# Kernel tuning notes

Hardware: AMD Instinct MI355X
Metric: run time of the kernel (lower is better)

Reference implementation:

```python
import jax, jax.numpy as jnp
import numpy as np

N_NODES = 50000
N_EDGES = 800000
IN_DIM = 256
HID = 64
HEADS = [4, 4, 1]
N_CLASSES = 16
SLOPE = 0.2


def mish(x):
    return x * jnp.tanh(jax.nn.softplus(x))


def gat_conv(x, src, dst, W, attn_l, attn_r, bias, res_W, n_heads, d_out, act):
    """DGL GATConv (feat_drop=attn_drop=0, residual=True, bias=True).
    x: (N, F_in); src/dst: (E,) edge endpoints; message flows src -> dst.
    """
    N = x.shape[0]
    feat = (x @ W).reshape(N, n_heads, d_out)            # (N, H, D)
    el = jnp.sum(feat * attn_l, axis=-1)                 # (N, H)
    er = jnp.sum(feat * attn_r, axis=-1)                 # (N, H)
    e = jax.nn.leaky_relu(el[src] + er[dst], SLOPE)      # (E, H)
    # segment softmax over incoming edges of each dst node
    emax = jax.ops.segment_max(e, dst, num_segments=N)   # (N, H)
    ee = jnp.exp(e - emax[dst])                          # (E, H)
    denom = jax.ops.segment_sum(ee, dst, num_segments=N) # (N, H)
    a = ee / denom[dst]                                  # (E, H)
    # weighted scatter-aggregate of source features
    rst = jax.ops.segment_sum(feat[src] * a[:, :, None], dst, num_segments=N)  # (N, H, D)
    # residual: identity if F_in == H*D else linear projection (DGL semantics)
    if res_W is None:
        res = x.reshape(N, n_heads, d_out)
    else:
        res = (x @ res_W).reshape(N, n_heads, d_out)
    rst = rst + res + bias.reshape(1, n_heads, d_out)
    if act:
        rst = mish(rst)
    return rst


def setup_inputs() -> dict:
    key = jax.random.key(0)
    ks = jax.random.split(key, 16)
    x = jax.random.normal(ks[0], (N_NODES, IN_DIM), dtype=jnp.float32)
    src = jax.random.randint(ks[1], (N_EDGES,), 0, N_NODES, dtype=jnp.int32)
    dst = jax.random.randint(ks[2], (N_EDGES,), 0, N_NODES, dtype=jnp.int32)
    s = 0.1
    # layer 0: 256 -> 4 heads x 64
    W0 = jax.random.normal(ks[3], (IN_DIM, HEADS[0] * HID), jnp.float32) * s
    al0 = jax.random.normal(ks[4], (HEADS[0], HID), jnp.float32) * s
    ar0 = jax.random.normal(ks[5], (HEADS[0], HID), jnp.float32) * s
    b0 = jnp.zeros((HEADS[0] * HID,), jnp.float32)
    # layer 1: 256 -> 4 heads x 64
    W1 = jax.random.normal(ks[6], (HEADS[0] * HID, HEADS[1] * HID), jnp.float32) * s
    al1 = jax.random.normal(ks[7], (HEADS[1], HID), jnp.float32) * s
    ar1 = jax.random.normal(ks[8], (HEADS[1], HID), jnp.float32) * s
    b1 = jnp.zeros((HEADS[1] * HID,), jnp.float32)
    # output layer: 256 -> 1 head x 16 (residual needs a linear projection)
    W2 = jax.random.normal(ks[9], (HEADS[1] * HID, HEADS[2] * N_CLASSES), jnp.float32) * s
    al2 = jax.random.normal(ks[10], (HEADS[2], N_CLASSES), jnp.float32) * s
    ar2 = jax.random.normal(ks[11], (HEADS[2], N_CLASSES), jnp.float32) * s
    b2 = jnp.zeros((HEADS[2] * N_CLASSES,), jnp.float32)
    resW2 = jax.random.normal(ks[12], (HEADS[1] * HID, HEADS[2] * N_CLASSES), jnp.float32) * s
    return {"x": x, "src": src, "dst": dst,
            "W0": W0, "al0": al0, "ar0": ar0, "b0": b0,
            "W1": W1, "al1": al1, "ar1": ar1, "b1": b1,
            "W2": W2, "al2": al2, "ar2": ar2, "b2": b2, "resW2": resW2}


def reference(x, src, dst, W0, al0, ar0, b0, W1, al1, ar1, b1, W2, al2, ar2, b2, resW2):
    N = x.shape[0]
    h = gat_conv(x, src, dst, W0, al0, ar0, b0, None, HEADS[0], HID, True).reshape(N, -1)
    h = gat_conv(h, src, dst, W1, al1, ar1, b1, None, HEADS[1], HID, True).reshape(N, -1)
    logits = gat_conv(h, src, dst, W2, al2, ar2, b2, resW2, HEADS[2], N_CLASSES, False).mean(axis=1)
    return logits
```

## Files before the change

### kernel.cpp

```cpp
#include <hip/hip_runtime.h>
#include <cmath>
#include <type_traits>

typedef __bf16 bf16;
typedef __attribute__((ext_vector_type(8))) __bf16 bf16x8;
typedef __attribute__((ext_vector_type(4))) __bf16 bf16x4;
typedef __attribute__((ext_vector_type(4))) float f32x4;

__device__ __forceinline__ unsigned f2s(float x) {
    unsigned u = __float_as_uint(x);
    return (u & 0x80000000u) ? ~u : (u | 0x80000000u);
}
__device__ __forceinline__ float s2f(unsigned s) {
    return (s & 0x80000000u) ? __uint_as_float(s & 0x7FFFFFFFu)
                             : __uint_as_float(~s);
}

__global__ void prep_weights_kernel(const float* __restrict__ W0, const float* __restrict__ W1,
                                    const float* __restrict__ W2, const float* __restrict__ rW2,
                                    bf16* __restrict__ Wt0, bf16* __restrict__ Wt1,
                                    bf16* __restrict__ Bct) {
    const int idx = blockIdx.x * blockDim.x + threadIdx.x;
    if (idx < 65536) {
        const int k = idx >> 8, m = idx & 255;
        Wt0[m * 256 + k] = (bf16)W0[idx];
        Wt1[m * 256 + k] = (bf16)W1[idx];
    }
    if (idx < 8192) {
        const int m = idx >> 8, k = idx & 255;
        const float v = (m < 16) ? W2[k * 16 + m] : rW2[k * 16 + (m - 16)];
        Bct[idx] = (bf16)v;
    }
}

template <typename AT>
__global__ __launch_bounds__(256) void gemm_mfma_bf16(const AT* __restrict__ A,
                                                      const bf16* __restrict__ Bt,
                                                      bf16* __restrict__ Fb, int N) {
    constexpr int K = 256, BM = 128, BK = 32;
    constexpr int LDA = BK + 8;
    __shared__ bf16 As[BM * LDA];
    __shared__ bf16 Bs[BM * LDA];

    const int tid = threadIdx.x;
    const int wave = tid >> 6, lane = tid & 63;
    const int quad = lane >> 4, l16 = lane & 15;
    const int rowBase = blockIdx.y * BM;
    const int colBase = blockIdx.x * BM;
    const int m_base = (wave >> 1) * 64, n_base = (wave & 1) * 64;

    f32x4 acc[4][4] = {};

    const int sr = tid >> 1;
    const int seg = (tid & 1) << 4;

    for (int k0 = 0; k0 < K; k0 += BK) {
        {
            const int gr = rowBase + sr;
            if constexpr (std::is_same<AT, float>::value) {
                float4 f0 = {0,0,0,0}, f1 = {0,0,0,0}, f2 = {0,0,0,0}, f3 = {0,0,0,0};
                if (gr < N) {
                    const float4* Ag = (const float4*)(A + (long)gr * K + k0 + seg);
                    f0 = Ag[0]; f1 = Ag[1]; f2 = Ag[2]; f3 = Ag[3];
                }
                bf16x8 p0, p1;
                p0[0] = (bf16)f0.x; p0[1] = (bf16)f0.y; p0[2] = (bf16)f0.z; p0[3] = (bf16)f0.w;
                p0[4] = (bf16)f1.x; p0[5] = (bf16)f1.y; p0[6] = (bf16)f1.z; p0[7] = (bf16)f1.w;
                p1[0] = (bf16)f2.x; p1[1] = (bf16)f2.y; p1[2] = (bf16)f2.z; p1[3] = (bf16)f2.w;
                p1[4] = (bf16)f3.x; p1[5] = (bf16)f3.y; p1[6] = (bf16)f3.z; p1[7] = (bf16)f3.w;
                *(bf16x8*)&As[sr * LDA + seg] = p0;
                *(bf16x8*)&As[sr * LDA + seg + 8] = p1;
            } else {
                bf16x8 p0 = {}, p1 = {};
                if (gr < N) {
                    const bf16x8* Ag = (const bf16x8*)(A + (long)gr * K + k0 + seg);
                    p0 = Ag[0]; p1 = Ag[1];
                }
                *(bf16x8*)&As[sr * LDA + seg] = p0;
                *(bf16x8*)&As[sr * LDA + seg + 8] = p1;
            }
        }
        {
            const bf16x8* Bg = (const bf16x8*)(Bt + (long)(colBase + sr) * K + k0 + seg);
            *(bf16x8*)&Bs[sr * LDA + seg] = Bg[0];
            *(bf16x8*)&Bs[sr * LDA + seg + 8] = Bg[1];
        }
        __syncthreads();

        bf16x8 af[4], bfr[4];
#pragma unroll
        for (int mi = 0; mi < 4; mi++)
            af[mi] = *(const bf16x8*)&As[(m_base + mi * 16 + l16) * LDA + quad * 8];
#pragma unroll
        for (int ni = 0; ni < 4; ni++)
            bfr[ni] = *(const bf16x8*)&Bs[(n_base + ni * 16 + l16) * LDA + quad * 8];
#pragma unroll
        for (int mi = 0; mi < 4; mi++)
#pragma unroll
            for (int ni = 0; ni < 4; ni++)
                acc[mi][ni] = __builtin_amdgcn_mfma_f32_16x16x32_bf16(af[mi], bfr[ni], acc[mi][ni], 0, 0, 0);
        __syncthreads();
    }

#pragma unroll
    for (int mi = 0; mi < 4; mi++) {
#pragma unroll
        for (int r = 0; r < 4; r++) {
            const int grow = rowBase + m_base + mi * 16 + quad * 4 + r;
            if (grow < N) {
#pragma unroll
                for (int ni = 0; ni < 4; ni++) {
                    Fb[(long)grow * 256 + colBase + n_base + ni * 16 + l16] = (bf16)acc[mi][ni][r];
                }
            }
        }
    }
}

__global__ __launch_bounds__(256) void gemm_mfma_n32(const bf16* __restrict__ A,
                                                     const bf16* __restrict__ Bt,
                                                     float* __restrict__ C, int N) {
    constexpr int K = 256, BM = 128, BK = 32;
    constexpr int LDA = BK + 8;
    __shared__ bf16 As[BM * LDA];
    __shared__ bf16 Bs[32 * LDA];

    const int tid = threadIdx.x;
    const int wave = tid >> 6, lane = tid & 63;
    const int quad = lane >> 4, l16 = lane & 15;
    const int rowBase = blockIdx.x * BM;
    const int m_base = (wave >> 1) * 64, n_base = (wave & 1) * 16;

    f32x4 acc[4] = {};

    const int sr = tid >> 1;
    const int seg = (tid & 1) << 4;

    for (int k0 = 0; k0 < K; k0 += BK) {
        {
            const int gr = rowBase + sr;
            bf16x8 p0 = {}, p1 = {};
            if (gr < N) {
                const bf16x8* Ag = (const bf16x8*)(A + (long)gr * K + k0 + seg);
                p0 = Ag[0]; p1 = Ag[1];
            }
            *(bf16x8*)&As[sr * LDA + seg] = p0;
            *(bf16x8*)&As[sr * LDA + seg + 8] = p1;
        }
        if (tid < 64) {
            const int br = tid >> 1;
            const bf16x8* Bg = (const bf16x8*)(Bt + br * K + k0 + seg);
            *(bf16x8*)&Bs[br * LDA + seg] = Bg[0];
            *(bf16x8*)&Bs[br * LDA + seg + 8] = Bg[1];
        }
        __syncthreads();

        const bf16x8 bfr = *(const bf16x8*)&Bs[(n_base + l16) * LDA + quad * 8];
#pragma unroll
        for (int mi = 0; mi < 4; mi++) {
            const bf16x8 af = *(const bf16x8*)&As[(m_base + mi * 16 + l16) * LDA + quad * 8];
            acc[mi] = __builtin_amdgcn_mfma_f32_16x16x32_bf16(af, bfr, acc[mi], 0, 0, 0);
        }
        __syncthreads();
    }

#pragma unroll
    for (int mi = 0; mi < 4; mi++) {
#pragma unroll
        for (int r = 0; r < 4; r++) {
            const int grow = rowBase + m_base + mi * 16 + quad * 4 + r;
            if (grow < N) C[(long)grow * 32 + n_base + l16] = acc[mi][r];
        }
    }
}

__global__ void el_er_node_kernel(const bf16* __restrict__ feat,
                                  const float* __restrict__ al, const float* __restrict__ ar,
                                  float* __restrict__ el, float* __restrict__ er, int N) {
    const int wid = (blockIdx.x * blockDim.x + threadIdx.x) >> 6;
    const int lane = threadIdx.x & 63;
    if (wid >= N) return;
    const bf16x4 f = ((const bf16x4*)feat)[(long)wid * 64 + lane];
    const float4 a = ((const float4*)al)[lane];
    const float4 b = ((const float4*)ar)[lane];
    const float f0 = (float)f[0], f1 = (float)f[1], f2 = (float)f[2], f3 = (float)f[3];
    float vl = f0 * a.x + f1 * a.y + f2 * a.z + f3 * a.w;
    float vr = f0 * b.x + f1 * b.y + f2 * b.z + f3 * b.w;
#pragma unroll
    for (int off = 1; off < 16; off <<= 1) {
        vl += __shfl_xor(vl, off);
        vr += __shfl_xor(vr, off);
    }
    if ((lane & 15) == 0) {
        const int h = lane >> 4;
        el[wid * 4 + h] = vl;
        er[wid * 4 + h] = vr;
    }
}

__global__ void el_er_strided16(const float* __restrict__ feat, int stride,
                                const float* __restrict__ al, const float* __restrict__ ar,
                                float* __restrict__ el, float* __restrict__ er, int N) {
    const int wid = (blockIdx.x * blockDim.x + threadIdx.x) >> 6;
    const int lane = threadIdx.x & 63;
    if (wid >= N) return;
    float vl = 0.f, vr = 0.f;
    if (lane < 16) {
        float f = feat[(long)wid * stride + lane];
        vl = f * al[lane];
        vr = f * ar[lane];
    }
#pragma unroll
    for (int off = 1; off < 16; off <<= 1) {
        vl += __shfl_xor(vl, off);
        vr += __shfl_xor(vr, off);
    }
    if (lane == 0) { el[wid] = vl; er[wid] = vr; }
}

__global__ void elmax4_kernel(const float4* __restrict__ el4, unsigned* __restrict__ elmax_u, int n4) {
    __shared__ float4 sm[256];
    float4 m = {-INFINITY, -INFINITY, -INFINITY, -INFINITY};
    for (int i = blockIdx.x * blockDim.x + threadIdx.x; i < n4; i += gridDim.x * blockDim.x) {
        const float4 v = el4[i];
        m.x = fmaxf(m.x, v.x); m.y = fmaxf(m.y, v.y);
        m.z = fmaxf(m.z, v.z); m.w = fmaxf(m.w, v.w);
    }
    sm[threadIdx.x] = m;
    __syncthreads();
    for (int off = 128; off > 0; off >>= 1) {
        if (threadIdx.x < off) {
            float4 o = sm[threadIdx.x + off];
            float4 c = sm[threadIdx.x];
            c.x = fmaxf(c.x, o.x); c.y = fmaxf(c.y, o.y);
            c.z = fmaxf(c.z, o.z); c.w = fmaxf(c.w, o.w);
            sm[threadIdx.x] = c;
        }
        __syncthreads();
    }
    if (threadIdx.x == 0) {
        const float4 r = sm[0];
        atomicMax(&elmax_u[0], f2s(r.x));
        atomicMax(&elmax_u[1], f2s(r.y));
        atomicMax(&elmax_u[2], f2s(r.z));
        atomicMax(&elmax_u[3], f2s(r.w));
    }
}


__global__ void count_deg_kernel(const int* __restrict__ dst, int* __restrict__ deg, int E) {
    const int e = blockIdx.x * blockDim.x + threadIdx.x;
    if (e >= E) return;
    atomicAdd(&deg[dst[e]], 1);
}

__global__ void scan_block_kernel(const int* __restrict__ deg, int* __restrict__ scanned,
                                  int* __restrict__ block_sums, int N) {
    __shared__ int smem[256];
    const int tid = threadIdx.x;
    const int base = blockIdx.x * 1024 + tid * 4;
    int v[4];
#pragma unroll
    for (int i = 0; i < 4; i++) v[i] = (base + i < N) ? deg[base + i] : 0;
    const int tsum = v[0] + v[1] + v[2] + v[3];
    smem[tid] = tsum;
    __syncthreads();
    int acc = tsum;
    for (int off = 1; off < 256; off <<= 1) {
        const int t = (tid >= off) ? smem[tid - off] : 0;
        __syncthreads();
        acc += t;
        smem[tid] = acc;
        __syncthreads();
    }
    if (tid == 255) block_sums[blockIdx.x] = acc;
    int run = acc - tsum;
#pragma unroll
    for (int i = 0; i < 4; i++) {
        if (base + i < N) scanned[base + i] = run;
        run += v[i];
    }
}

__global__ void scan_sums_kernel(int* __restrict__ block_sums, unsigned* __restrict__ elmax_u, int nb) {
    const int tid = threadIdx.x;
    if (tid < 12) elmax_u[tid] = f2s(-INFINITY);
    const int orig = (tid < nb) ? block_sums[tid] : 0;
    int v = orig;
#pragma unroll
    for (int off = 1; off < 64; off <<= 1) {
        const int t = __shfl_up(v, off);
        if (tid >= off) v += t;
    }
    if (tid < nb) block_sums[tid] = v - orig;
}

__global__ void apply_offsets_kernel(const int* __restrict__ scanned, const int* __restrict__ block_sums,
                                     int* __restrict__ row_ptr, int* __restrict__ cursor, int N, int E) {
    const int i = blockIdx.x * blockDim.x + threadIdx.x;
    if (i < N) {
        const int v = scanned[i] + block_sums[i >> 10];
        row_ptr[i] = v;
        cursor[i] = v;
    }
    if (i == 0) row_ptr[N] = E;
}

__global__ void scatter_kernel(const int* __restrict__ src, const int* __restrict__ dst,
                               int* __restrict__ cursor, int* __restrict__ csr_src, int E) {
    const int e = blockIdx.x * blockDim.x + threadIdx.x;
    if (e >= E) return;
    const int pos = atomicAdd(&cursor[dst[e]], 1);
    csr_src[pos] = src[e];
}

template <int H, int D, bool ACT, typename RT, typename OT>
__global__ void gat_aggregate_wave(const int* __restrict__ row_ptr, const int* __restrict__ csr_src,
                                   const float* __restrict__ el, const float* __restrict__ er,
                                   const unsigned* __restrict__ elmax_u,
                                   const bf16* __restrict__ feat,
                                   const RT* __restrict__ res, const float* __restrict__ bias,
                                   OT* __restrict__ out, int N) {
    constexpr int C = H * D;
    constexpr int V = C / 4;
    const int wave = threadIdx.x >> 6;
    const int lane = threadIdx.x & 63;
    int n = blockIdx.x * (blockDim.x >> 6) + wave;
    if (n >= N) return;
    n = __builtin_amdgcn_readfirstlane(n);
    const int h = lane >> 4;
    const bf16x4* feat4 = (const bf16x4*)feat;

    const float erd = er[n * H + h];
    float sh = s2f(elmax_u[h]) + erd;
    sh = (sh >= 0.f) ? sh : 0.2f * sh;

    float4 acc = {0.f, 0.f, 0.f, 0.f};
    float l = 0.f;
    int p = row_ptr[n];
    const int pend = row_ptr[n + 1];
    for (; p + 4 <= pend; p += 4) {
        const int s0 = csr_src[p + 0];
        const int s1 = csr_src[p + 1];
        const int s2 = csr_src[p + 2];
        const int s3 = csr_src[p + 3];
        float e0 = el[s0 * H + h] + erd;
        float e1 = el[s1 * H + h] + erd;
        float e2 = el[s2 * H + h] + erd;
        float e3 = el[s3 * H + h] + erd;
        e0 = (e0 >= 0.f) ? e0 : 0.2f * e0;
        e1 = (e1 >= 0.f) ? e1 : 0.2f * e1;
        e2 = (e2 >= 0.f) ? e2 : 0.2f * e2;
        e3 = (e3 >= 0.f) ? e3 : 0.2f * e3;
        const float w0 = __expf(e0 - sh);
        const float w1 = __expf(e1 - sh);
        const float w2 = __expf(e2 - sh);
        const float w3 = __expf(e3 - sh);
        const bf16x4 f0 = feat4[(long)s0 * V + lane];
        const bf16x4 f1 = feat4[(long)s1 * V + lane];
        const bf16x4 f2 = feat4[(long)s2 * V + lane];
        const bf16x4 f3 = feat4[(long)s3 * V + lane];
        l += w0 + w1 + w2 + w3;
        acc.x += w0 * (float)f0[0] + w1 * (float)f1[0] + w2 * (float)f2[0] + w3 * (float)f3[0];
        acc.y += w0 * (float)f0[1] + w1 * (float)f1[1] + w2 * (float)f2[1] + w3 * (float)f3[1];
        acc.z += w0 * (float)f0[2] + w1 * (float)f1[2] + w2 * (float)f2[2] + w3 * (float)f3[2];
        acc.w += w0 * (float)f0[3] + w1 * (float)f1[3] + w2 * (float)f2[3] + w3 * (float)f3[3];
    }
    for (; p < pend; ++p) {
        const int s = csr_src[p];
        float e = el[s * H + h] + erd;
        e = (e >= 0.f) ? e : 0.2f * e;
        const float w = __expf(e - sh);
        const bf16x4 f = feat4[(long)s * V + lane];
        l += w;
        acc.x += w * (float)f[0];
        acc.y += w * (float)f[1];
        acc.z += w * (float)f[2];
        acc.w += w * (float)f[3];
    }
    const float inv = (l > 0.f) ? 1.f / l : 0.f;
    acc.x *= inv; acc.y *= inv; acc.z *= inv; acc.w *= inv;

    float4 r;
    if constexpr (std::is_same<RT, float>::value) {
        r = ((const float4*)res)[(long)n * V + lane];
    } else {
        const bf16x4 rb = ((const bf16x4*)res)[(long)n * V + lane];
        r = make_float4((float)rb[0], (float)rb[1], (float)rb[2], (float)rb[3]);
    }
    const float4 bb = ((const float4*)bias)[lane];
    float v[4] = {acc.x + r.x + bb.x, acc.y + r.y + bb.y,
                  acc.z + r.z + bb.z, acc.w + r.w + bb.w};
    if (ACT) {
#pragma unroll
        for (int i = 0; i < 4; i++) {
            const float sp = (v[i] > 20.f) ? v[i] : log1pf(expf(v[i]));
            v[i] = v[i] * tanhf(sp);
        }
    }
    if constexpr (std::is_same<OT, float>::value) {
        float4 o = {v[0], v[1], v[2], v[3]};
        ((float4*)out)[(long)n * V + lane] = o;
    } else {
        bf16x4 o;
        o[0] = (bf16)v[0]; o[1] = (bf16)v[1]; o[2] = (bf16)v[2]; o[3] = (bf16)v[3];
        ((bf16x4*)out)[(long)n * V + lane] = o;
    }
}

template <bool ACT, int NPB>
__global__ void gat_aggregate_small(const int* __restrict__ row_ptr, const int* __restrict__ csr_src,
                                    const float* __restrict__ el, const float* __restrict__ er,
                                    const unsigned* __restrict__ elmax_u,
                                    const float* __restrict__ feat, int fstride,
                                    const float* __restrict__ res, int rstride,
                                    const float* __restrict__ bias, float* __restrict__ out, int N) {
    constexpr int C = 16;
    const int local = threadIdx.x % C;
    const int n = blockIdx.x * NPB + threadIdx.x / C;
    if (n >= N) return;
    const float mx = fmaxf(fmaxf(s2f(elmax_u[8]), s2f(elmax_u[9])),
                           fmaxf(s2f(elmax_u[10]), s2f(elmax_u[11])));
    const float erd = er[n];
    float sh = mx + erd;
    sh = (sh >= 0.f) ? sh : 0.2f * sh;

    float acc = 0.f, l = 0.f;
    int p = row_ptr[n];
    const int pend = row_ptr[n + 1];
    for (; p + 4 <= pend; p += 4) {
        const int s0 = csr_src[p + 0];
        const int s1 = csr_src[p + 1];
        const int s2 = csr_src[p + 2];
        const int s3 = csr_src[p + 3];
        float e0 = el[s0] + erd, e1 = el[s1] + erd, e2 = el[s2] + erd, e3 = el[s3] + erd;
        e0 = (e0 >= 0.f) ? e0 : 0.2f * e0;
        e1 = (e1 >= 0.f) ? e1 : 0.2f * e1;
        e2 = (e2 >= 0.f) ? e2 : 0.2f * e2;
        e3 = (e3 >= 0.f) ? e3 : 0.2f * e3;
        const float w0 = __expf(e0 - sh);
        const float w1 = __expf(e1 - sh);
        const float w2 = __expf(e2 - sh);
        const float w3 = __expf(e3 - sh);
        l += w0 + w1 + w2 + w3;
        acc += w0 * feat[(long)s0 * fstride + local] + w1 * feat[(long)s1 * fstride + local]
             + w2 * feat[(long)s2 * fstride + local] + w3 * feat[(long)s3 * fstride + local];
    }
    for (; p < pend; ++p) {
        const int s = csr_src[p];
        float e = el[s] + erd;
        e = (e >= 0.f) ? e : 0.2f * e;
        const float w = __expf(e - sh);
        l += w;
        acc += w * feat[(long)s * fstride + local];
    }
    const float inv = (l > 0.f) ? 1.f / l : 0.f;
    float v = acc * inv + res[(long)n * rstride + local] + bias[local];
    if (ACT) {
        const float sp = (v > 20.f) ? v : log1pf(expf(v));
        v = v * tanhf(sp);
    }
    out[(long)n * C + local] = v;
}


static inline int cdiv(long a, long b) { return (int)((a + b - 1) / b); }

extern "C" void kernel_launch(void* const* d_in, const int* in_sizes, int n_in,
                              void* d_out, int out_size, void* d_ws, size_t ws_size,
                              hipStream_t stream) {
    const float* x   = (const float*)d_in[0];
    const int*   src = (const int*)d_in[1];
    const int*   dst = (const int*)d_in[2];
    const float* W0  = (const float*)d_in[3];
    const float* al0 = (const float*)d_in[4];
    const float* ar0 = (const float*)d_in[5];
    const float* b0  = (const float*)d_in[6];
    const float* W1  = (const float*)d_in[7];
    const float* al1 = (const float*)d_in[8];
    const float* ar1 = (const float*)d_in[9];
    const float* b1  = (const float*)d_in[10];
    const float* W2  = (const float*)d_in[11];
    const float* al2 = (const float*)d_in[12];
    const float* ar2 = (const float*)d_in[13];
    const float* b2  = (const float*)d_in[14];
    const float* rW2 = (const float*)d_in[15];
    float* out = (float*)d_out;

    const int N = in_sizes[0] / 256;
    const int E = in_sizes[1];

    bf16* Wt0    = (bf16*)d_ws;
    bf16* Wt1    = Wt0 + 65536;
    bf16* Bct    = Wt1 + 65536;
    bf16* Fb     = Bct + 8192;
    bf16* Hb     = Fb + (long)N * 256;
    float* F2    = (float*)(Hb + (long)N * 256);
    float* el    = F2 + (long)N * 32;
    float* er    = el + (long)N * 4;
    unsigned* elmax_u = (unsigned*)(er + (long)N * 4);
    int* deg     = (int*)(elmax_u + 12);
    int* scanned = deg + N;
    int* bsums   = scanned + N;
    int* row_ptr = bsums + 64;
    int* cursor  = row_ptr + N + 1;
    int* csr_src = cursor + N;

    const int THREADS = 256;
    const int NB = cdiv(N, 1024);
    dim3 mfma_grid(2, cdiv(N, 128));

    prep_weights_kernel<<<cdiv(65536, THREADS), THREADS, 0, stream>>>(W0, W1, W2, rW2, Wt0, Wt1, Bct);
    hipMemsetAsync(deg, 0, (size_t)N * 4, stream);
    count_deg_kernel<<<cdiv(E, THREADS), THREADS, 0, stream>>>(dst, deg, E);
    scan_block_kernel<<<NB, 256, 0, stream>>>(deg, scanned, bsums, N);
    scan_sums_kernel<<<1, 64, 0, stream>>>(bsums, elmax_u, NB);
    apply_offsets_kernel<<<cdiv(N, THREADS), THREADS, 0, stream>>>(scanned, bsums, row_ptr, cursor, N, E);
    scatter_kernel<<<cdiv(E, THREADS), THREADS, 0, stream>>>(src, dst, cursor, csr_src, E);

    gemm_mfma_bf16<float><<<mfma_grid, 256, 0, stream>>>(x, Wt0, Fb, N);
    el_er_node_kernel<<<cdiv(N, 4), 256, 0, stream>>>(Fb, al0, ar0, el, er, N);
    elmax4_kernel<<<64, 256, 0, stream>>>((const float4*)el, elmax_u, N);
    gat_aggregate_wave<4, 64, true, float, bf16><<<cdiv(N, 4), 256, 0, stream>>>(
        row_ptr, csr_src, el, er, elmax_u, Fb, x, b0, Hb, N);

    gemm_mfma_bf16<bf16><<<mfma_grid, 256, 0, stream>>>(Hb, Wt1, Fb, N);
    el_er_node_kernel<<<cdiv(N, 4), 256, 0, stream>>>(Fb, al1, ar1, el, er, N);
    elmax4_kernel<<<64, 256, 0, stream>>>((const float4*)el, elmax_u + 4, N);
    gat_aggregate_wave<4, 64, true, bf16, bf16><<<cdiv(N, 4), 256, 0, stream>>>(
        row_ptr, csr_src, el, er, elmax_u + 4, Fb, Hb, b1, Hb, N);

    gemm_mfma_n32<<<cdiv(N, 128), 256, 0, stream>>>(Hb, Bct, F2, N);
    el_er_strided16<<<cdiv(N, 4), 256, 0, stream>>>(F2, 32, al2, ar2, el, er, N);
    elmax4_kernel<<<64, 256, 0, stream>>>((const float4*)el, elmax_u + 8, N / 4);
    gat_aggregate_small<false, 16><<<cdiv(N, 16), 256, 0, stream>>>(row_ptr, csr_src, el, er, elmax_u,
                                                                    F2, 32, F2 + 16, 32, b2, out, N);
}
```

Measured before the change: 478.4 us.

## Split edges across half-waves in GAT aggregation and use fast exp2/mish

The 256-channel aggregation now has each half-wave process alternate edges with 8-wide bf16 loads, then combines the two halves with a cross-lane shuffle. The 16-class output layer moves from 16 lanes per node to one wave per node, with four edge slots per wave reduced by shuffles. Leaky-relu plus exp is folded into a single exp2 over a max of two FMAs, and mish uses a closed-form rational expression with a hardware reciprocal. These changes target gather latency and transcendental cost. They add shuffle reductions and use 32-bit unsigned byte offsets, plus approximate math that may change rounding slightly.

```diff
diff --git a/kernel.cpp b/kernel.cpp
--- a/kernel.cpp
+++ b/kernel.cpp
@@ -14,6 +14,13 @@
 __device__ __forceinline__ float s2f(unsigned s) {
     return (s & 0x80000000u) ? __uint_as_float(s & 0x7FFFFFFFu)
                              : __uint_as_float(~s);
+}
+
+__device__ __forceinline__ float fast_mish(float x) {
+    const float t = __expf(fminf(x, 32.f));
+    const float num = fmaf(t, t, t + t);
+    const float den = num + 2.f;
+    return x * num * __builtin_amdgcn_rcpf(den);
 }
 
 __global__ void prep_weights_kernel(const float* __restrict__ W0, const float* __restrict__ W1,
@@ -321,146 +328,168 @@
                                    const bf16* __restrict__ feat,
                                    const RT* __restrict__ res, const float* __restrict__ bias,
                                    OT* __restrict__ out, int N) {
-    constexpr int C = H * D;
-    constexpr int V = C / 4;
+    static_assert(H == 4 && D == 64, "layout hardcoded for C=256");
     const int wave = threadIdx.x >> 6;
     const int lane = threadIdx.x & 63;
     int n = blockIdx.x * (blockDim.x >> 6) + wave;
     if (n >= N) return;
     n = __builtin_amdgcn_readfirstlane(n);
-    const int h = lane >> 4;
-    const bf16x4* feat4 = (const bf16x4*)feat;
+    const int sel = lane >> 5;
+    const int hl = lane & 31;
+    const int h = hl >> 3;
 
     const float erd = er[n * H + h];
     float sh = s2f(elmax_u[h]) + erd;
-    sh = (sh >= 0.f) ? sh : 0.2f * sh;
-
-    float4 acc = {0.f, 0.f, 0.f, 0.f};
+    sh = fmaxf(sh, 0.2f * sh);
+    constexpr float L2E = 1.4426950408889634f;
+    const float C1 = (erd - sh) * L2E;
+    const float C2 = fmaf(0.2f, erd, -sh) * L2E;
+
+    const char* csrB = (const char*)csr_src;
+    const char* elB = (const char*)el;
+    const char* featB = (const char*)feat;
+    const unsigned hoff = (unsigned)(h << 2);
+    const unsigned coff = (unsigned)(hl << 4);
+    const unsigned selo = (unsigned)(sel << 2);
+
+    float acc[8] = {0.f, 0.f, 0.f, 0.f, 0.f, 0.f, 0.f, 0.f};
     float l = 0.f;
     int p = row_ptr[n];
     const int pend = row_ptr[n + 1];
+
+#define EDGE2(PP)                                                                  \
+    {                                                                              \
+        const int s_ = *(const int*)(csrB + ((unsigned)((PP) << 2) + selo));       \
+        const float ev_ = *(const float*)(elB + ((unsigned)(s_ << 4) + hoff));     \
+        const float w_ = __builtin_amdgcn_exp2f(                                   \
+            fmaxf(fmaf(ev_, L2E, C1), fmaf(ev_, 0.2f * L2E, C2)));                 \
+        const bf16x8 f_ = *(const bf16x8*)(featB + ((unsigned)(s_ << 9) + coff));  \
+        l += w_;                                                                   \
+        _Pragma("unroll") for (int i_ = 0; i_ < 8; i_++)                           \
+            acc[i_] = fmaf(w_, (float)f_[i_], acc[i_]);                            \
+    }
+
     for (; p + 4 <= pend; p += 4) {
-        const int s0 = csr_src[p + 0];
-        const int s1 = csr_src[p + 1];
-        const int s2 = csr_src[p + 2];
-        const int s3 = csr_src[p + 3];
-        float e0 = el[s0 * H + h] + erd;
-        float e1 = el[s1 * H + h] + erd;
-        float e2 = el[s2 * H + h] + erd;
-        float e3 = el[s3 * H + h] + erd;
-        e0 = (e0 >= 0.f) ? e0 : 0.2f * e0;
-        e1 = (e1 >= 0.f) ? e1 : 0.2f * e1;
-        e2 = (e2 >= 0.f) ? e2 : 0.2f * e2;
-        e3 = (e3 >= 0.f) ? e3 : 0.2f * e3;
-        const float w0 = __expf(e0 - sh);
-        const float w1 = __expf(e1 - sh);
-        const float w2 = __expf(e2 - sh);
-        const float w3 = __expf(e3 - sh);
-        const bf16x4 f0 = feat4[(long)s0 * V + lane];
-        const bf16x4 f1 = feat4[(long)s1 * V + lane];
-        const bf16x4 f2 = feat4[(long)s2 * V + lane];
-        const bf16x4 f3 = feat4[(long)s3 * V + lane];
-        l += w0 + w1 + w2 + w3;
-        acc.x += w0 * (float)f0[0] + w1 * (float)f1[0] + w2 * (float)f2[0] + w3 * (float)f3[0];
-        acc.y += w0 * (float)f0[1] + w1 * (float)f1[1] + w2 * (float)f2[1] + w3 * (float)f3[1];
-        acc.z += w0 * (float)f0[2] + w1 * (float)f1[2] + w2 * (float)f2[2] + w3 * (float)f3[2];
-        acc.w += w0 * (float)f0[3] + w1 * (float)f1[3] + w2 * (float)f2[3] + w3 * (float)f3[3];
-    }
-    for (; p < pend; ++p) {
-        const int s = csr_src[p];
-        float e = el[s * H + h] + erd;
-        e = (e >= 0.f) ? e : 0.2f * e;
-        const float w = __expf(e - sh);
-        const bf16x4 f = feat4[(long)s * V + lane];
-        l += w;
-        acc.x += w * (float)f[0];
-        acc.y += w * (float)f[1];
-        acc.z += w * (float)f[2];
-        acc.w += w * (float)f[3];
-    }
-    const float inv = (l > 0.f) ? 1.f / l : 0.f;
-    acc.x *= inv; acc.y *= inv; acc.z *= inv; acc.w *= inv;
+        EDGE2(p)
+        EDGE2(p + 2)
+    }
+    for (; p + 2 <= pend; p += 2) {
+        EDGE2(p)
+    }
+    if (p < pend) {
+        const int s_ = *(const int*)(csrB + (unsigned)(p << 2));
+        const float ev_ = *(const float*)(elB + ((unsigned)(s_ << 4) + hoff));
+        float w_ = __builtin_amdgcn_exp2f(
+            fmaxf(fmaf(ev_, L2E, C1), fmaf(ev_, 0.2f * L2E, C2)));
+        if (sel) w_ = 0.f;
+        const bf16x8 f_ = *(const bf16x8*)(featB + ((unsigned)(s_ << 9) + coff));
+        l += w_;
+#pragma unroll
+        for (int i_ = 0; i_ < 8; i_++) acc[i_] = fmaf(w_, (float)f_[i_], acc[i_]);
+    }
+#undef EDGE2
+
+    l += __shfl_xor(l, 32);
+#pragma unroll
+    for (int i = 0; i < 8; i++) acc[i] += __shfl_xor(acc[i], 32);
+    const float inv = (l > 0.f) ? __builtin_amdgcn_rcpf(l) : 0.f;
+
+    const float a0 = (sel ? acc[4] : acc[0]) * inv;
+    const float a1 = (sel ? acc[5] : acc[1]) * inv;
+    const float a2 = (sel ? acc[6] : acc[2]) * inv;
+    const float a3 = (sel ? acc[7] : acc[3]) * inv;
+    const unsigned ib = (unsigned)(sel << 2);
 
     float4 r;
     if constexpr (std::is_same<RT, float>::value) {
-        r = ((const float4*)res)[(long)n * V + lane];
+        r = *(const float4*)((const char*)res + ((size_t)n << 10) + (coff << 1) + (ib << 2));
     } else {
-        const bf16x4 rb = ((const bf16x4*)res)[(long)n * V + lane];
+        const bf16x4 rb = *(const bf16x4*)((const char*)res + ((size_t)n << 9) + coff + (ib << 1));
         r = make_float4((float)rb[0], (float)rb[1], (float)rb[2], (float)rb[3]);
     }
-    const float4 bb = ((const float4*)bias)[lane];
-    float v[4] = {acc.x + r.x + bb.x, acc.y + r.y + bb.y,
-                  acc.z + r.z + bb.z, acc.w + r.w + bb.w};
+    const float4 bb = *(const float4*)((const char*)bias + (coff << 1) + (ib << 2));
+    float v0 = a0 + r.x + bb.x;
+    float v1 = a1 + r.y + bb.y;
+    float v2 = a2 + r.z + bb.z;
+    float v3 = a3 + r.w + bb.w;
     if (ACT) {
-#pragma unroll
-        for (int i = 0; i < 4; i++) {
-            const float sp = (v[i] > 20.f) ? v[i] : log1pf(expf(v[i]));
-            v[i] = v[i] * tanhf(sp);
-        }
+        v0 = fast_mish(v0);
+        v1 = fast_mish(v1);
+        v2 = fast_mish(v2);
+        v3 = fast_mish(v3);
     }
     if constexpr (std::is_same<OT, float>::value) {
-        float4 o = {v[0], v[1], v[2], v[3]};
-        ((float4*)out)[(long)n * V + lane] = o;
+        float4 o = {v0, v1, v2, v3};
+        *(float4*)((char*)out + ((size_t)n << 10) + (coff << 1) + (ib << 2)) = o;
     } else {
         bf16x4 o;
-        o[0] = (bf16)v[0]; o[1] = (bf16)v[1]; o[2] = (bf16)v[2]; o[3] = (bf16)v[3];
-        ((bf16x4*)out)[(long)n * V + lane] = o;
-    }
-}
-
-template <bool ACT, int NPB>
-__global__ void gat_aggregate_small(const int* __restrict__ row_ptr, const int* __restrict__ csr_src,
-                                    const float* __restrict__ el, const float* __restrict__ er,
-                                    const unsigned* __restrict__ elmax_u,
-                                    const float* __restrict__ feat, int fstride,
-                                    const float* __restrict__ res, int rstride,
-                                    const float* __restrict__ bias, float* __restrict__ out, int N) {
-    constexpr int C = 16;
-    const int local = threadIdx.x % C;
-    const int n = blockIdx.x * NPB + threadIdx.x / C;
+        o[0] = (bf16)v0; o[1] = (bf16)v1; o[2] = (bf16)v2; o[3] = (bf16)v3;
+        *(bf16x4*)((char*)out + ((size_t)n << 9) + coff + (ib << 1)) = o;
+    }
+}
+
+__global__ void gat_aggregate_small16(const int* __restrict__ row_ptr, const int* __restrict__ csr_src,
+                                      const float* __restrict__ el, const float* __restrict__ er,
+                                      const unsigned* __restrict__ elmax_u,
+                                      const float* __restrict__ F2, const float* __restrict__ bias,
+                                      float* __restrict__ out, int N) {
+    const int wave = threadIdx.x >> 6;
+    const int lane = threadIdx.x & 63;
+    int n = blockIdx.x * (blockDim.x >> 6) + wave;
     if (n >= N) return;
+    n = __builtin_amdgcn_readfirstlane(n);
+    const int slot = lane >> 4;
+    const int c = lane & 15;
+
     const float mx = fmaxf(fmaxf(s2f(elmax_u[8]), s2f(elmax_u[9])),
                            fmaxf(s2f(elmax_u[10]), s2f(elmax_u[11])));
     const float erd = er[n];
     float sh = mx + erd;
-    sh = (sh >= 0.f) ? sh : 0.2f * sh;
+    sh = fmaxf(sh, 0.2f * sh);
+    constexpr float L2E = 1.4426950408889634f;
+    const float C1 = (erd - sh) * L2E;
+    const float C2 = fmaf(0.2f, erd, -sh) * L2E;
+
+    const char* csrB = (const char*)csr_src;
+    const char* elB = (const char*)el;
+    const char* fB = (const char*)F2;
+    const unsigned co = (unsigned)(c << 2);
+    const unsigned so = (unsigned)(slot << 2);
 
     float acc = 0.f, l = 0.f;
     int p = row_ptr[n];
     const int pend = row_ptr[n + 1];
     for (; p + 4 <= pend; p += 4) {
-        const int s0 = csr_src[p + 0];
-        const int s1 = csr_src[p + 1];
-        const int s2 = csr_src[p + 2];
-        const int s3 = csr_src[p + 3];
-        float e0 = el[s0] + erd, e1 = el[s1] + erd, e2 = el[s2] + erd, e3 = el[s3] + erd;
-        e0 = (e0 >= 0.f) ? e0 : 0.2f * e0;
-        e1 = (e1 >= 0.f) ? e1 : 0.2f * e1;
-        e2 = (e2 >= 0.f) ? e2 : 0.2f * e2;
-        e3 = (e3 >= 0.f) ? e3 : 0.2f * e3;
-        const float w0 = __expf(e0 - sh);
-        const float w1 = __expf(e1 - sh);
-        const float w2 = __expf(e2 - sh);
-        const float w3 = __expf(e3 - sh);
-        l += w0 + w1 + w2 + w3;
-        acc += w0 * feat[(long)s0 * fstride + local] + w1 * feat[(long)s1 * fstride + local]
-             + w2 * feat[(long)s2 * fstride + local] + w3 * feat[(long)s3 * fstride + local];
-    }
-    for (; p < pend; ++p) {
-        const int s = csr_src[p];
-        float e = el[s] + erd;
-        e = (e >= 0.f) ? e : 0.2f * e;
-        const float w = __expf(e - sh);
-        l += w;
-        acc += w * feat[(long)s * fstride + local];
-    }
-    const float inv = (l > 0.f) ? 1.f / l : 0.f;
-    float v = acc * inv + res[(long)n * rstride + local] + bias[local];
-    if (ACT) {
-        const float sp = (v > 20.f) ? v : log1pf(expf(v));
-        v = v * tanhf(sp);
-    }
-    out[(long)n * C + local] = v;
+        const int s_ = *(const int*)(csrB + ((unsigned)(p << 2) + so));
+        const float ev_ = *(const float*)(elB + (unsigned)(s_ << 2));
+        const float w_ = __builtin_amdgcn_exp2f(
+            fmaxf(fmaf(ev_, L2E, C1), fmaf(ev_, 0.2f * L2E, C2)));
+        const float f_ = *(const float*)(fB + ((unsigned)(s_ << 7) + co));
+        l += w_;
+        acc = fmaf(w_, f_, acc);
+    }
+    if (p < pend) {
+        const int q = p + slot;
+        const bool valid = q < pend;
+        const int qi = valid ? q : p;
+        const int s_ = *(const int*)(csrB + (unsigned)(qi << 2));
+        const float ev_ = *(const float*)(elB + (unsigned)(s_ << 2));
+        float w_ = __builtin_amdgcn_exp2f(
+            fmaxf(fmaf(ev_, L2E, C1), fmaf(ev_, 0.2f * L2E, C2)));
+        if (!valid) w_ = 0.f;
+        const float f_ = *(const float*)(fB + ((unsigned)(s_ << 7) + co));
+        l += w_;
+        acc = fmaf(w_, f_, acc);
+    }
+    l += __shfl_xor(l, 16);
+    l += __shfl_xor(l, 32);
+    acc += __shfl_xor(acc, 16);
+    acc += __shfl_xor(acc, 32);
+    const float inv = (l > 0.f) ? __builtin_amdgcn_rcpf(l) : 0.f;
+    if (lane < 16) {
+        const float rv = *(const float*)(fB + ((unsigned)(n << 7) + 64u + co));
+        out[(long)n * 16 + c] = fmaf(acc, inv, rv + bias[c]);
+    }
 }
 
 
@@ -533,6 +562,6 @@
     gemm_mfma_n32<<<cdiv(N, 128), 256, 0, stream>>>(Hb, Bct, F2, N);
     el_er_strided16<<<cdiv(N, 4), 256, 0, stream>>>(F2, 32, al2, ar2, el, er, N);
     elmax4_kernel<<<64, 256, 0, stream>>>((const float4*)el, elmax_u + 8, N / 4);
-    gat_aggregate_small<false, 16><<<cdiv(N, 16), 256, 0, stream>>>(row_ptr, csr_src, el, er, elmax_u,
-                                                                    F2, 32, F2 + 16, 32, b2, out, N);
-}
+    gat_aggregate_small16<<<cdiv(N, 4), 256, 0, stream>>>(row_ptr, csr_src, el, er, elmax_u,
+                                                          F2, b2, out, N);
+}
```

Result: faster. 458.3 us (-4.2%).
